# Kernel optimization log

Hardware: AMD Instinct MI355X
Metric: run time of the kernel (lower is better)

Reference implementation:

```python
import jax, jax.numpy as jnp
import numpy as np

B, S, H, NH, T = 128, 512, 768, 8, 20
HD = H // NH


def setup_inputs() -> dict:
    key = jax.random.key(0)
    ks = jax.random.split(key, 16)
    f32 = jnp.float32
    def W(i, *shape):
        return jax.random.normal(ks[i], shape, f32) * 0.02
    inp = {}
    inp["ehs"] = jax.random.normal(ks[0], (B, S, H), f32)
    inp["relevance"] = jax.random.uniform(ks[1], (B, 1), dtype=f32)
    inp["threshold"] = jnp.array([0.5], f32)
    # text_to_caption_proj: Linear, LeakyReLU, LayerNorm, Linear
    inp["tW1"] = W(2, H, H); inp["tb1"] = jnp.zeros((H,), f32)
    inp["tg"] = jnp.ones((H,), f32); inp["tbe"] = jnp.zeros((H,), f32)
    inp["tW2"] = W(3, H, H); inp["tb2"] = jnp.zeros((H,), f32)
    # image_to_caption_proj
    inp["iW1"] = W(4, H, H); inp["ib1"] = jnp.zeros((H,), f32)
    inp["ig"] = jnp.ones((H,), f32); inp["ibe"] = jnp.zeros((H,), f32)
    inp["iW2"] = W(5, H, H); inp["ib2"] = jnp.zeros((H,), f32)
    # nn.MultiheadAttention packed in_proj [3H,H] + out_proj [H,H], x2
    inp["taWin"] = W(6, 3 * H, H); inp["taBin"] = jnp.zeros((3 * H,), f32)
    inp["taWout"] = W(7, H, H); inp["taBout"] = jnp.zeros((H,), f32)
    inp["iaWin"] = W(8, 3 * H, H); inp["iaBin"] = jnp.zeros((3 * H,), f32)
    inp["iaWout"] = W(9, H, H); inp["iaBout"] = jnp.zeros((H,), f32)
    # length_adapter: Linear, LayerNorm, ReLU
    inp["laW"] = W(10, H, H); inp["laB"] = jnp.zeros((H,), f32)
    inp["laG"] = jnp.ones((H,), f32); inp["laBe"] = jnp.zeros((H,), f32)
    # quality_estimator: Linear(H,H/2), LayerNorm, ReLU, Linear(H/2,1), Sigmoid
    inp["qW1"] = W(11, H // 2, H); inp["qB1"] = jnp.zeros((H // 2,), f32)
    inp["qG"] = jnp.ones((H // 2,), f32); inp["qBe"] = jnp.zeros((H // 2,), f32)
    inp["qW2"] = W(12, 1, H // 2); inp["qB2"] = jnp.zeros((1,), f32)
    # masks: first half = text tokens, second half = image tokens; no valid
    # image caption => torch loop gives batch_max_length=0 => target_length=20
    pos = jnp.arange(S)
    inp["sentence_mask"] = jnp.tile((pos < S // 2).astype(jnp.int32)[None], (B, 1))
    inp["image_mask"] = jnp.tile((pos >= S // 2).astype(jnp.int32)[None], (B, 1))
    inp["image_caption_mask"] = jnp.zeros((B, S), jnp.int32)
    inp["image_caption_valid"] = jnp.zeros((B,), jnp.int32)
    return inp


def _ln(x, g, b, eps=1e-5):
    m = x.mean(-1, keepdims=True)
    v = ((x - m) ** 2).mean(-1, keepdims=True)
    return (x - m) / jnp.sqrt(v + eps) * g + b


def _mha(q, k, v, Win, bIn, Wout, bOut, key_pad):
    # torch nn.MultiheadAttention, batch_first=True
    Wq, Wk, Wv = jnp.split(Win, 3, axis=0)
    bq, bk, bv = jnp.split(bIn, 3, axis=0)
    def heads(x, Wp, bp):  # [B,L,H] -> [B,NH,L,HD]
        return (x @ Wp.T + bp).reshape(x.shape[0], x.shape[1], NH, HD).transpose(0, 2, 1, 3)
    qh, kh, vh = heads(q, Wq, bq), heads(k, Wk, bk), heads(v, Wv, bv)
    scores = jnp.einsum('bhqd,bhkd->bhqk', qh, kh) / jnp.sqrt(jnp.float32(HD))
    scores = jnp.where(key_pad[:, None, None, :], -1e9, scores)
    attn = jax.nn.softmax(scores, axis=-1)
    out = jnp.einsum('bhqk,bhkd->bhqd', attn, vh)
    out = out.transpose(0, 2, 1, 3).reshape(q.shape[0], q.shape[1], H)
    return out @ Wout.T + bOut


def _sinusoid_pe():
    # vectorized replacement of the scalar double for-loop
    pos = jnp.arange(T, dtype=jnp.float32)[:, None]            # [T,1]
    i = jnp.arange(0, H, 2, dtype=jnp.float32)                 # [H/2]
    ang = pos / (10000.0 ** (i / H))                           # [T,H/2]
    pe = jnp.zeros((T, H), jnp.float32)
    pe = pe.at[:, 0::2].set(jnp.sin(ang)).at[:, 1::2].set(jnp.cos(ang))
    return pe[None]  # [1,T,H]


def reference(ehs, relevance, threshold,
              tW1, tb1, tg, tbe, tW2, tb2,
              iW1, ib1, ig, ibe, iW2, ib2,
              taWin, taBin, taWout, taBout,
              iaWin, iaBin, iaWout, iaBout,
              laW, laB, laG, laBe,
              qW1, qB1, qG, qBe, qW2, qB2,
              sentence_mask, image_mask, image_caption_mask, image_caption_valid):
    sm = sentence_mask.astype(jnp.float32)[..., None]   # [B,S,1]
    im = image_mask.astype(jnp.float32)[..., None]
    text_emb = ehs * sm
    image_emb = ehs * im
    # image_caption_valid is all False => target_length = min(20, max_length-2) = T (static)
    text_len = jnp.clip(sm.sum(axis=1), 1e-9)            # [B,1]
    img_len = jnp.clip(im.sum(axis=1), 1e-9)
    text_pooled = (text_emb * sm).sum(axis=1) / text_len  # mask applied twice, as in torch
    image_pooled = (image_emb * im).sum(axis=1) / img_len
    def proj(x, W1, b1, g, be, W2, b2):
        h = jax.nn.leaky_relu(x @ W1.T + b1, 0.01)
        return _ln(h, g, be) @ W2.T + b2
    text_seed = proj(text_pooled, tW1, tb1, tg, tbe, tW2, tb2)
    image_seed = proj(image_pooled, iW1, ib1, ig, ibe, iW2, ib2)
    alpha = relevance                                     # relevance_score provided
    caption_seed = alpha * image_seed + (1.0 - alpha) * text_seed
    query = caption_seed[:, None, :] + _sinusoid_pe()     # [B,T,H]
    text_cap = _mha(query, text_emb, text_emb, taWin, taBin, taWout, taBout, sentence_mask == 0)
    image_cap = _mha(query, image_emb, image_emb, iaWin, iaBin, iaWout, iaBout, image_mask == 0)
    beta = relevance[:, :, None]                          # [B,1,1]
    cap = beta * image_cap + (1.0 - beta) * text_cap
    cap = jax.nn.relu(_ln(cap @ laW.T + laB, laG, laBe))  # length_adapter
    m = cap.mean(axis=1)
    h = jax.nn.relu(_ln(m @ qW1.T + qB1, qG, qBe))
    quality = jax.nn.sigmoid(h @ qW2.T + qB2)             # [B,1]
    return cap, quality
```

## Files before the change

### kernel.cpp

```cpp
#include <hip/hip_runtime.h>
#include <hip/hip_bf16.h>
#include <math.h>

#define B_  128
#define S_  512
#define H_  768
#define NH_ 8
#define T_  20
#define HD_ 96

typedef unsigned short u16;
typedef unsigned int   u32;

typedef __attribute__((ext_vector_type(8))) short bhalf8;
typedef __attribute__((ext_vector_type(4))) float f32x4;

union U8 { bhalf8 s; u32 u[4]; };

__device__ __forceinline__ f32x4 mfma16(bhalf8 a, bhalf8 b, f32x4 c){
  return __builtin_amdgcn_mfma_f32_16x16x32_bf16(a, b, c, 0, 0, 0);
}
__device__ __forceinline__ u32 cvtpk(float lo, float hi){
  u32 r; asm volatile("v_cvt_pk_bf16_f32 %0, %1, %2" : "=v"(r) : "v"(lo), "v"(hi));
  return r;
}
__device__ __forceinline__ float wsum(float v){
  #pragma unroll
  for(int o=32;o;o>>=1) v += __shfl_xor(v,o);
  return v;
}
__device__ __forceinline__ u16 f2bf(float f){
  u32 u = __float_as_uint(f);
  u32 r = (u + 0x7fffu + ((u>>16)&1u)) >> 16;
  return (u16)r;
}
__device__ __forceinline__ float bf2f(u32 bits){
  return __uint_as_float(bits<<16);
}

__global__ void k_cvt(const float* __restrict__ src, u16* __restrict__ dst, int n2){
  int i = blockIdx.x*256 + threadIdx.x;
  if(i < n2){
    u32 r = cvtpk(src[2*i], src[2*i+1]);
    *(u32*)(dst + 2*i) = r;
  }
}

__global__ __launch_bounds__(256) void k_prep(const float* __restrict__ ehs,
                                              u16* __restrict__ ehs_b,
                                              u16* __restrict__ ehsT){
  int blk = blockIdx.x;
  int b  = blk / 96;
  int r  = blk % 96;
  int sb = r / 12, hb = r % 12;
  int s0 = sb*64, h0 = hb*64;
  __shared__ float tile[64][65];
  int t = threadIdx.x;
  const float* src = ehs + ((size_t)b*S_ + s0)*H_ + h0;
  #pragma unroll
  for(int p2=0;p2<4;p2++){
    int row = p2*16 + (t>>4);
    int c4  = (t&15)*4;
    float4 v = *(const float4*)(src + (size_t)row*H_ + c4);
    tile[row][c4+0]=v.x; tile[row][c4+1]=v.y; tile[row][c4+2]=v.z; tile[row][c4+3]=v.w;
    u32 lo = cvtpk(v.x, v.y), hi2 = cvtpk(v.z, v.w);
    u32* dst = (u32*)(ehs_b + ((size_t)b*S_ + s0 + row)*H_ + h0 + c4);
    dst[0]=lo; dst[1]=hi2;
  }
  __syncthreads();
  #pragma unroll
  for(int p2=0;p2<4;p2++){
    int hr = p2*16 + (t>>4);
    int sg = (t&15)*4;
    float a0 = tile[sg+0][hr], a1 = tile[sg+1][hr];
    float a2 = tile[sg+2][hr], a3 = tile[sg+3][hr];
    u32 lo = cvtpk(a0,a1), hi2 = cvtpk(a2,a3);
    u32* dst = (u32*)(ehsT + ((size_t)b*H_ + h0 + hr)*S_ + s0 + sg);
    dst[0]=lo; dst[1]=hi2;
  }
}

__global__ void k_wkt(const float* __restrict__ taWin, const float* __restrict__ iaWin,
                      u16* __restrict__ WkT){
  int blk = blockIdx.x; int mha = blk/576; int t = blk%576;
  const float* Wk = (mha? iaWin : taWin) + (size_t)H_*H_;
  int bx = t%24, by = t/24;
  __shared__ float tile[32][33];
  int tx = threadIdx.x & 31, ty = threadIdx.x >> 5;
  for(int rr=ty; rr<32; rr+=8) tile[rr][tx] = Wk[(size_t)(by*32+rr)*H_ + bx*32+tx];
  __syncthreads();
  u16* dst = WkT + (size_t)mha*H_*H_;
  for(int rr=ty; rr<32; rr+=8) dst[(size_t)(bx*32+rr)*H_ + by*32+tx] = f2bf(tile[tx][rr]);
}

__global__ void k_pool(const float* __restrict__ ehs, const int* __restrict__ sm,
                       const int* __restrict__ im, u16* __restrict__ pt_b, u16* __restrict__ pi_b){
  int blk = blockIdx.x; int b = blk/3; int c0 = (blk%3)*256;
  int tid = threadIdx.x;
  __shared__ float smf[S_], imf[S_];
  for(int s=tid;s<S_;s+=256){ smf[s]=(float)sm[b*S_+s]; imf[s]=(float)im[b*S_+s]; }
  __syncthreads();
  float tl=0.f, il=0.f;
  for(int s=0;s<S_;s++){ tl+=smf[s]; il+=imf[s]; }
  tl = fmaxf(tl, 1e-9f); il = fmaxf(il, 1e-9f);
  int col = c0 + tid;
  const float* base = ehs + (size_t)b*S_*H_ + col;
  float ts=0.f, is=0.f;
  for(int s=0;s<S_;s++){
    float a = base[(size_t)s*H_];
    ts += a*smf[s];
    is += a*imf[s];
  }
  pt_b[b*H_+col] = f2bf(ts/tl);
  pi_b[b*H_+col] = f2bf(is/il);
}

__global__ __launch_bounds__(512) void k_seed(const u16* __restrict__ x_b,
                                              const u16* __restrict__ W1_b,
                                              const float* __restrict__ b1,
                                              const float* __restrict__ g,
                                              const float* __restrict__ be,
                                              const u16* __restrict__ W2_b,
                                              const float* __restrict__ b2,
                                              float* __restrict__ out){
  int row0 = blockIdx.x*16;
  int tid = threadIdx.x, lane = tid&63, w = tid>>6;
  __shared__ u16 ln[16][772];
  f32x4 acc[6];
  #pragma unroll
  for(int j=0;j<6;j++) acc[j] = (f32x4){0.f,0.f,0.f,0.f};
  for(int kt=0;kt<24;kt++){
    int ko = kt*32 + (lane>>4)*8;
    bhalf8 a = *(const bhalf8*)(x_b + (size_t)(row0 + (lane&15))*H_ + ko);
    bhalf8 bb[6];
    #pragma unroll
    for(int j=0;j<6;j++){
      int row = (w*6+j)*16 + (lane&15);
      bb[j] = *(const bhalf8*)(W1_b + (size_t)row*H_ + ko);
    }
    #pragma unroll
    for(int j=0;j<6;j++) acc[j] = mfma16(a, bb[j], acc[j]);
  }
  #pragma unroll
  for(int j=0;j<6;j++){
    int c = (w*6+j)*16 + (lane&15);
    float bv = b1[c];
    #pragma unroll
    for(int rr=0;rr<4;rr++){
      int r = (lane>>4)*4 + rr;
      float v = acc[j][rr] + bv;
      ln[r][c] = f2bf((v>=0.f)? v : 0.01f*v);
    }
  }
  __syncthreads();
  for(int ri=0; ri<2; ri++){
    int r = w*2 + ri;
    float v[12]; float s = 0.f;
    #pragma unroll
    for(int i=0;i<12;i++){ v[i] = bf2f(ln[r][lane + 64*i]); s += v[i]; }
    s = wsum(s);
    float mean = s/(float)H_;
    float pv = 0.f;
    #pragma unroll
    for(int i=0;i<12;i++){ float d = v[i]-mean; pv += d*d; }
    pv = wsum(pv);
    float rstd = rsqrtf(pv/(float)H_ + 1e-5f);
    #pragma unroll
    for(int i=0;i<12;i++){
      int c = lane + 64*i;
      ln[r][c] = f2bf((v[i]-mean)*rstd*g[c] + be[c]);
    }
  }
  __syncthreads();
  f32x4 o[6];
  #pragma unroll
  for(int j=0;j<6;j++) o[j] = (f32x4){0.f,0.f,0.f,0.f};
  for(int kt=0;kt<24;kt++){
    int ko = kt*32 + (lane>>4)*8;
    bhalf8 a = *(const bhalf8*)(&ln[lane&15][ko]);
    bhalf8 bb[6];
    #pragma unroll
    for(int j=0;j<6;j++){
      int row = (w*6+j)*16 + (lane&15);
      bb[j] = *(const bhalf8*)(W2_b + (size_t)row*H_ + ko);
    }
    #pragma unroll
    for(int j=0;j<6;j++) o[j] = mfma16(a, bb[j], o[j]);
  }
  #pragma unroll
  for(int j=0;j<6;j++){
    int c = (w*6+j)*16 + (lane&15);
    float bv = b2[c];
    #pragma unroll
    for(int rr=0;rr<4;rr++){
      int r = (lane>>4)*4 + rr;
      out[(size_t)(row0 + r)*H_ + c] = o[j][rr] + bv;
    }
  }
}

__global__ void k_query(const float* __restrict__ st, const float* __restrict__ si,
                        const float* __restrict__ rel, u16* __restrict__ query_b){
  int b = blockIdx.x; int tid = threadIdx.x;
  float a = rel[b];
  const float c = 9.210340371976184f/(float)H_;
  for(int t=0;t<32;t++){
    for(int h=tid;h<H_;h+=256){
      float val = 0.f;
      if(t < T_){
        float ang = (float)t * __expf(-(float)(h & ~1) * c);
        float pe  = (h&1)? __cosf(ang) : __sinf(ang);
        val = a*si[b*H_+h] + (1.f-a)*st[b*H_+h] + pe;
      }
      query_b[(size_t)b*32*H_ + t*H_ + h] = f2bf(val);
    }
  }
}

__global__ __launch_bounds__(512) void k_qh(const u16* __restrict__ query_b,
                                            const u16* __restrict__ Wq_b,
                                            const float* __restrict__ taBin,
                                            const float* __restrict__ iaBin,
                                            u16* __restrict__ qh_b){
  int gb = blockIdx.x; int b = gb>>1, mha = gb&1;
  int tid = threadIdx.x, lane = tid&63, w = tid>>6;
  const u16* Q  = query_b + (size_t)b*32*H_;
  const u16* Wq = Wq_b + (size_t)mha*H_*H_;
  const float* bIn = mha? iaBin : taBin;
  u16* out = qh_b + (size_t)gb*32*H_;
  f32x4 acc[2][6];
  #pragma unroll
  for(int i=0;i<2;i++)
    #pragma unroll
    for(int j=0;j<6;j++) acc[i][j] = (f32x4){0.f,0.f,0.f,0.f};
  for(int kt=0;kt<24;kt++){
    int ko = kt*32 + (lane>>4)*8;
    bhalf8 a[2];
    #pragma unroll
    for(int mt=0;mt<2;mt++)
      a[mt] = *(const bhalf8*)(Q + (size_t)(mt*16 + (lane&15))*H_ + ko);
    bhalf8 bb[6];
    #pragma unroll
    for(int j=0;j<6;j++){
      int row = (w*6+j)*16 + (lane&15);
      bb[j] = *(const bhalf8*)(Wq + (size_t)row*H_ + ko);
    }
    #pragma unroll
    for(int mt=0;mt<2;mt++)
      #pragma unroll
      for(int j=0;j<6;j++) acc[mt][j] = mfma16(a[mt], bb[j], acc[mt][j]);
  }
  #pragma unroll
  for(int mt=0;mt<2;mt++)
    #pragma unroll
    for(int j=0;j<6;j++){
      int col = (w*6+j)*16 + (lane&15);
      float bq = bIn[col];
      #pragma unroll
      for(int rr=0;rr<4;rr++){
        int row = mt*16 + (lane>>4)*4 + rr;
        out[(size_t)row*H_ + col] = f2bf(acc[mt][j][rr] + bq);
      }
    }
}

__global__ __launch_bounds__(512) void k_u(const u16* __restrict__ qh_b,
                                           const u16* __restrict__ WkT,
                                           const float* __restrict__ taBin,
                                           const float* __restrict__ iaBin,
                                           u16* __restrict__ U_b,
                                           float* __restrict__ bias_ws){
  int gb = blockIdx.x; int mha = gb&1;
  int tid = threadIdx.x, lane = tid&63, w = tid>>6;
  const u16* qh = qh_b + (size_t)gb*32*H_;
  const u16* Wk = WkT + (size_t)mha*H_*H_;
  u16* Up = U_b + (size_t)gb*160*H_;
  const float rscale = 0.10206207261596577f;
  for(int h=0; h<8; h++){
    int hd0 = h*HD_;
    for(int jn=0; jn<6; jn++){
      int nb = (w*6+jn)*16 + (lane&15);
      bhalf8 bb[3];
      #pragma unroll
      for(int kt=0;kt<3;kt++)
        bb[kt] = *(const bhalf8*)(Wk + (size_t)nb*H_ + hd0 + kt*32 + (lane>>4)*8);
      #pragma unroll
      for(int mt=0; mt<2; mt++){
        bhalf8 a[3];
        #pragma unroll
        for(int kt=0;kt<3;kt++){
          int trow = mt*16 + (lane&15);
          a[kt] = *(const bhalf8*)(qh + (size_t)trow*H_ + hd0 + kt*32 + (lane>>4)*8);
        }
        f32x4 acc = (f32x4){0.f,0.f,0.f,0.f};
        #pragma unroll
        for(int kt=0;kt<3;kt++) acc = mfma16(a[kt], bb[kt], acc);
        #pragma unroll
        for(int rr=0;rr<4;rr++){
          int trow = mt*16 + (lane>>4)*4 + rr;
          if(trow < T_)
            Up[(size_t)(h*T_+trow)*H_ + nb] = f2bf(acc[rr]*rscale);
        }
      }
    }
  }
  if(tid < 160){
    int h = tid/T_, t = tid%T_; int hd0 = h*HD_;
    const float* bIn = mha? iaBin : taBin;
    float p = 0.f;
    for(int d=0; d<HD_; d++)
      p += bf2f(qh[(size_t)t*H_ + hd0 + d]) * bIn[H_ + hd0 + d];
    bias_ws[gb*160 + tid] = p*rscale;
  }
}

__global__ __launch_bounds__(512,4) void k_scores2(const u16* __restrict__ ehs_b,
                                                   const u16* __restrict__ U_b,
                                                   const float* __restrict__ bias_ws,
                                                   const int* __restrict__ smask,
                                                   const int* __restrict__ imask,
                                                   u16* __restrict__ P_b){
  int g = blockIdx.x;
  int x = g & 7, sl = g >> 3;
  int b = x*16 + (sl>>2);
  int var = sl & 3; int mha = var>>1, rhalf = var&1;
  int gb = 2*b + mha;
  const int* msk = mha? imask : smask;
  int tid = threadIdx.x, lane = tid&63, w = tid>>6;
  int rbase = rhalf*80;
  __shared__ float sbias[80];
  __shared__ float pmax[80][8];
  __shared__ float psum[80][8];
  __shared__ float mfin[80], sinv[80];
  __shared__ u16 pst[16][520];
  if(tid < 80) sbias[tid] = bias_ws[gb*160 + rbase + tid];
  __syncthreads();
  const u16* Ub = U_b + (size_t)gb*160*H_;
  const u16* Eb = ehs_b + (size_t)b*S_*H_;
  bool mk[4];
  #pragma unroll
  for(int j=0;j<4;j++) mk[j] = msk[b*S_ + w*64 + j*16 + (lane&15)] != 0;

  f32x4 acc[5][4];
  #pragma unroll
  for(int i=0;i<5;i++)
    #pragma unroll
    for(int j=0;j<4;j++) acc[i][j] = (f32x4){0.f,0.f,0.f,0.f};
  for(int kt=0;kt<24;kt++){
    int ko = kt*32 + (lane>>4)*8;
    bhalf8 a[5];
    #pragma unroll
    for(int i=0;i<5;i++)
      a[i] = *(const bhalf8*)(Ub + (size_t)(rbase + i*16 + (lane&15))*H_ + ko);
    bhalf8 bb[4];
    #pragma unroll
    for(int j=0;j<4;j++)
      bb[j] = *(const bhalf8*)(Eb + (size_t)(w*64 + j*16 + (lane&15))*H_ + ko);
    #pragma unroll
    for(int i=0;i<5;i++)
      #pragma unroll
      for(int j=0;j<4;j++) acc[i][j] = mfma16(a[i], bb[j], acc[i][j]);
  }
  #pragma unroll
  for(int i=0;i<5;i++)
    #pragma unroll
    for(int rr=0;rr<4;rr++){
      int row = i*16 + (lane>>4)*4 + rr;
      float bias = sbias[row];
      float vmax = -3e38f;
      #pragma unroll
      for(int j=0;j<4;j++){
        float v = acc[i][j][rr] + bias;
        acc[i][j][rr] = v;
        if(mk[j]) vmax = fmaxf(vmax, v);
      }
      #pragma unroll
      for(int o=1;o<16;o<<=1) vmax = fmaxf(vmax, __shfl_xor(vmax,o));
      if((lane&15)==0) pmax[row][w] = vmax;
    }
  __syncthreads();
  if(tid < 80){
    float m = pmax[tid][0];
    #pragma unroll
    for(int ww=1;ww<8;ww++) m = fmaxf(m, pmax[tid][ww]);
    mfin[tid] = m;
  }
  __syncthreads();
  #pragma unroll
  for(int i=0;i<5;i++)
    #pragma unroll
    for(int rr=0;rr<4;rr++){
      int row = i*16 + (lane>>4)*4 + rr;
      float m = mfin[row];
      float ssum = 0.f;
      #pragma unroll
      for(int j=0;j<4;j++){
        float e = mk[j]? __expf(acc[i][j][rr] - m) : 0.f;
        acc[i][j][rr] = e;
        ssum += e;
      }
      #pragma unroll
      for(int o=1;o<16;o<<=1) ssum += __shfl_xor(ssum,o);
      if((lane&15)==0) psum[row][w] = ssum;
    }
  __syncthreads();
  if(tid < 80){
    float ss = 0.f;
    #pragma unroll
    for(int ww=0;ww<8;ww++) ss += psum[tid][ww];
    sinv[tid] = 1.f/ss;
  }
  __syncthreads();
  u16* Pp = P_b + (size_t)gb*160*S_ + (size_t)rbase*S_;
  for(int i=0;i<5;i++){
    #pragma unroll
    for(int rr=0;rr<4;rr++){
      int r16 = (lane>>4)*4 + rr;
      float inv = sinv[i*16 + r16];
      #pragma unroll
      for(int j=0;j<4;j++){
        int col = w*64 + j*16 + (lane&15);
        pst[r16][col] = f2bf(acc[i][j][rr]*inv);
      }
    }
    __syncthreads();
    for(int e=tid; e<16*256; e+=512){
      int r16 = e>>8, c = e&255;
      u32 v = *(const u32*)&pst[r16][2*c];
      *(u32*)(Pp + (size_t)(i*16 + r16)*S_ + 2*c) = v;
    }
    __syncthreads();
  }
}

__global__ __launch_bounds__(512) void k_ctx2(const u16* __restrict__ ehsT,
                                              const u16* __restrict__ P_b,
                                              u16* __restrict__ ctx_b){
  int blk = blockIdx.x; int b = blk>>1, nh = blk&1;
  int tid = threadIdx.x, lane = tid&63, w = tid>>6;
  __shared__ u16 ct[80][392];
  int nbase = nh*384 + w*48;
  for(int mha=0; mha<2; mha++){
    const u16* Pp = P_b + (size_t)(2*b+mha)*160*S_;
    f32x4 acc[10][3];
    #pragma unroll
    for(int i=0;i<10;i++)
      #pragma unroll
      for(int j=0;j<3;j++) acc[i][j] = (f32x4){0.f,0.f,0.f,0.f};
    for(int kt=0;kt<16;kt++){
      int ko = kt*32 + (lane>>4)*8;
      bhalf8 bb[3];
      #pragma unroll
      for(int t2=0;t2<3;t2++){
        int n = nbase + t2*16 + (lane&15);
        bb[t2] = *(const bhalf8*)(ehsT + ((size_t)b*H_ + n)*S_ + ko);
      }
      bhalf8 a[10];
      #pragma unroll
      for(int i=0;i<10;i++){
        int row = i*16 + (lane&15);
        a[i] = *(const bhalf8*)(Pp + (size_t)row*S_ + ko);
      }
      #pragma unroll
      for(int i=0;i<10;i++)
        #pragma unroll
        for(int t2=0;t2<3;t2++) acc[i][t2] = mfma16(a[i], bb[t2], acc[i][t2]);
    }
    u16* Cp = ctx_b + (size_t)(2*b+mha)*160*H_ + nh*384;
    #pragma unroll
    for(int half=0; half<2; half++){
      __syncthreads();
      #pragma unroll
      for(int i=0;i<5;i++)
        #pragma unroll
        for(int t2=0;t2<3;t2++)
          #pragma unroll
          for(int rr=0;rr<4;rr++){
            int rloc = i*16 + (lane>>4)*4 + rr;
            int cl = w*48 + t2*16 + (lane&15);
            ct[rloc][cl] = f2bf(acc[half*5+i][t2][rr]);
          }
      __syncthreads();
      for(int e=tid; e<80*192; e+=512){
        int r = e/192, c2 = (e%192)*2;
        u32 v = (u32)ct[r][c2] | ((u32)ct[r][c2+1]<<16);
        *(u32*)(Cp + (size_t)(half*80 + r)*H_ + c2) = v;
      }
    }
    __syncthreads();
  }
}

__global__ __launch_bounds__(512) void k_out(const u16* __restrict__ ctx_b,
                                             const u16* __restrict__ Wv_b,
                                             const u16* __restrict__ Wo_b,
                                             const float* __restrict__ taBin,
                                             const float* __restrict__ iaBin,
                                             float* __restrict__ out_t,
                                             float* __restrict__ out_i){
  int gb = blockIdx.x; int b = gb>>1, mha = gb&1;
  int tid = threadIdx.x, lane = tid&63, w = tid>>6;
  const float* bIn = mha? iaBin : taBin;
  const u16* Wv = Wv_b + (size_t)mha*H_*H_;
  const u16* Wo = Wo_b + (size_t)mha*H_*H_;
  const u16* Cp = ctx_b + (size_t)gb*160*H_;
  __shared__ u16 vt[32][784];
  int hd0 = w*HD_;
  {
    f32x4 acc[2][6];
    #pragma unroll
    for(int i=0;i<2;i++)
      #pragma unroll
      for(int j=0;j<6;j++) acc[i][j] = (f32x4){0.f,0.f,0.f,0.f};
    for(int kt=0;kt<24;kt++){
      int ko = kt*32 + (lane>>4)*8;
      bhalf8 a[2];
      #pragma unroll
      for(int mt=0;mt<2;mt++){
        int trow = mt*16 + (lane&15);
        a[mt] = *(const bhalf8*)(Cp + (size_t)(w*T_ + trow)*H_ + ko);
      }
      bhalf8 bb[6];
      #pragma unroll
      for(int j=0;j<6;j++){
        int row = hd0 + j*16 + (lane&15);
        bb[j] = *(const bhalf8*)(Wv + (size_t)row*H_ + ko);
      }
      #pragma unroll
      for(int mt=0;mt<2;mt++)
        #pragma unroll
        for(int j=0;j<6;j++) acc[mt][j] = mfma16(a[mt], bb[j], acc[mt][j]);
    }
    #pragma unroll
    for(int mt=0;mt<2;mt++)
      #pragma unroll
      for(int j=0;j<6;j++){
        int col = j*16 + (lane&15);
        float bv = bIn[2*H_ + hd0 + col];
        #pragma unroll
        for(int rr=0;rr<4;rr++){
          int trow = mt*16 + (lane>>4)*4 + rr;
          vt[trow][hd0 + col] = f2bf(acc[mt][j][rr] + bv);
        }
      }
  }
  __syncthreads();
  {
    f32x4 o[2][6];
    #pragma unroll
    for(int i=0;i<2;i++)
      #pragma unroll
      for(int j=0;j<6;j++) o[i][j] = (f32x4){0.f,0.f,0.f,0.f};
    for(int kt=0;kt<24;kt++){
      int ko = kt*32 + (lane>>4)*8;
      bhalf8 a[2];
      #pragma unroll
      for(int mt=0;mt<2;mt++)
        a[mt] = *(const bhalf8*)(&vt[mt*16 + (lane&15)][ko]);
      bhalf8 bb[6];
      #pragma unroll
      for(int j=0;j<6;j++){
        int row = (w*6+j)*16 + (lane&15);
        bb[j] = *(const bhalf8*)(Wo + (size_t)row*H_ + ko);
      }
      #pragma unroll
      for(int mt=0;mt<2;mt++)
        #pragma unroll
        for(int j=0;j<6;j++) o[mt][j] = mfma16(a[mt], bb[j], o[mt][j]);
    }
    float* op = (mha? out_i : out_t) + (size_t)b*T_*H_;
    #pragma unroll
    for(int mt=0;mt<2;mt++)
      #pragma unroll
      for(int j=0;j<6;j++){
        int col = (w*6+j)*16 + (lane&15);
        #pragma unroll
        for(int rr=0;rr<4;rr++){
          int trow = mt*16 + (lane>>4)*4 + rr;
          if(trow < T_) op[(size_t)trow*H_ + col] = o[mt][j][rr];
        }
      }
  }
}

__global__ void k_comb(const float* __restrict__ out_t, const float* __restrict__ out_i,
                       const float* __restrict__ taBout, const float* __restrict__ iaBout,
                       const float* __restrict__ rel, u16* __restrict__ comb_b){
  int bt = blockIdx.x; int b = bt/T_;
  float beta = rel[b];
  for(int h=threadIdx.x; h<H_; h+=256){
    float vt = out_t[(size_t)bt*H_+h] + taBout[h];
    float vi = out_i[(size_t)bt*H_+h] + iaBout[h];
    comb_b[(size_t)bt*H_+h] = f2bf(beta*vi + (1.f-beta)*vt);
  }
}

__global__ __launch_bounds__(512) void k_cap2(const u16* __restrict__ comb_b,
                                              const u16* __restrict__ laW_b,
                                              const float* __restrict__ laB,
                                              const float* __restrict__ laG,
                                              const float* __restrict__ laBe,
                                              float* __restrict__ cap){
  int blk = blockIdx.x; int row0 = blk*16;
  int tid = threadIdx.x, lane = tid&63, w = tid>>6;
  __shared__ float sy[16][776];
  f32x4 acc[6];
  #pragma unroll
  for(int j=0;j<6;j++) acc[j] = (f32x4){0.f,0.f,0.f,0.f};
  for(int kt=0;kt<24;kt++){
    int ko = kt*32 + (lane>>4)*8;
    bhalf8 a = *(const bhalf8*)(comb_b + (size_t)(row0 + (lane&15))*H_ + ko);
    bhalf8 bb[6];
    #pragma unroll
    for(int j=0;j<6;j++){
      int row = (w*6+j)*16 + (lane&15);
      bb[j] = *(const bhalf8*)(laW_b + (size_t)row*H_ + ko);
    }
    #pragma unroll
    for(int j=0;j<6;j++) acc[j] = mfma16(a, bb[j], acc[j]);
  }
  #pragma unroll
  for(int j=0;j<6;j++){
    int c = (w*6+j)*16 + (lane&15);
    float lb = laB[c];
    #pragma unroll
    for(int rr=0;rr<4;rr++){
      int r = (lane>>4)*4 + rr;
      sy[r][c] = acc[j][rr] + lb;
    }
  }
  __syncthreads();
  for(int ri=0; ri<2; ri++){
    int r = w*2 + ri;
    float v[12];
    float s = 0.f;
    #pragma unroll
    for(int i=0;i<12;i++){ v[i] = sy[r][lane + 64*i]; s += v[i]; }
    s = wsum(s);
    float mean = s/(float)H_;
    float pv = 0.f;
    #pragma unroll
    for(int i=0;i<12;i++){ float d = v[i]-mean; pv += d*d; }
    pv = wsum(pv);
    float rstd = rsqrtf(pv/(float)H_ + 1e-5f);
    float* cp = cap + (size_t)(row0 + r)*H_;
    #pragma unroll
    for(int i=0;i<12;i++){
      int c = lane + 64*i;
      float o = (v[i]-mean)*rstd*laG[c] + laBe[c];
      cp[c] = (o>0.f)? o : 0.f;
    }
  }
}

__global__ __launch_bounds__(512) void k_quality2(const float* __restrict__ cap,
                                                  const u16* __restrict__ qW1_b,
                                                  const float* __restrict__ qB1,
                                                  const float* __restrict__ qG,
                                                  const float* __restrict__ qBe,
                                                  const float* __restrict__ qW2,
                                                  const float* __restrict__ qB2,
                                                  float* __restrict__ outq){
  const int H2 = H_/2;
  int b0 = blockIdx.x*16;
  int tid = threadIdx.x, lane = tid&63, w = tid>>6;
  __shared__ u16 sm_a[16][772];
  __shared__ float sy[16][388];
  for(int e=tid; e<16*H_; e+=512){
    int r = e/H_, c = e%H_;
    const float* cp = cap + ((size_t)(b0+r)*T_)*H_ + c;
    float s = 0.f;
    #pragma unroll
    for(int t=0;t<T_;t++) s += cp[(size_t)t*H_];
    sm_a[r][c] = f2bf(s*(1.f/(float)T_));
  }
  __syncthreads();
  f32x4 acc[3];
  #pragma unroll
  for(int j=0;j<3;j++) acc[j] = (f32x4){0.f,0.f,0.f,0.f};
  for(int kt=0;kt<24;kt++){
    int ko = kt*32 + (lane>>4)*8;
    bhalf8 a = *(const bhalf8*)(&sm_a[lane&15][ko]);
    bhalf8 bb[3];
    #pragma unroll
    for(int j=0;j<3;j++){
      int row = (w*3+j)*16 + (lane&15);
      bb[j] = *(const bhalf8*)(qW1_b + (size_t)row*H_ + ko);
    }
    #pragma unroll
    for(int j=0;j<3;j++) acc[j] = mfma16(a, bb[j], acc[j]);
  }
  #pragma unroll
  for(int j=0;j<3;j++){
    int c = (w*3+j)*16 + (lane&15);
    float q1 = qB1[c];
    #pragma unroll
    for(int rr=0;rr<4;rr++){
      int r = (lane>>4)*4 + rr;
      sy[r][c] = acc[j][rr] + q1;
    }
  }
  __syncthreads();
  for(int ri=0; ri<2; ri++){
    int r = w*2 + ri;
    float v[6]; float s = 0.f;
    #pragma unroll
    for(int i=0;i<6;i++){ v[i] = sy[r][lane + 64*i]; s += v[i]; }
    s = wsum(s);
    float mean = s/(float)H2;
    float pv = 0.f;
    #pragma unroll
    for(int i=0;i<6;i++){ float d = v[i]-mean; pv += d*d; }
    pv = wsum(pv);
    float rstd = rsqrtf(pv/(float)H2 + 1e-5f);
    float dot = 0.f;
    #pragma unroll
    for(int i=0;i<6;i++){
      int c = lane + 64*i;
      float u = (v[i]-mean)*rstd*qG[c] + qBe[c];
      u = (u>0.f)? u : 0.f;
      dot += u*qW2[c];
    }
    dot = wsum(dot);
    if(lane==0){
      float z = dot + qB2[0];
      outq[b0+r] = 1.f/(1.f+__expf(-z));
    }
  }
}

extern "C" void kernel_launch(void* const* d_in, const int* in_sizes, int n_in,
                              void* d_out, int out_size, void* d_ws, size_t ws_size,
                              hipStream_t stream){
  const float* ehs    = (const float*)d_in[0];
  const float* rel    = (const float*)d_in[1];
  const float* tW1    = (const float*)d_in[3];
  const float* tb1    = (const float*)d_in[4];
  const float* tg     = (const float*)d_in[5];
  const float* tbe    = (const float*)d_in[6];
  const float* tW2    = (const float*)d_in[7];
  const float* tb2    = (const float*)d_in[8];
  const float* iW1    = (const float*)d_in[9];
  const float* ib1    = (const float*)d_in[10];
  const float* ig     = (const float*)d_in[11];
  const float* ibe    = (const float*)d_in[12];
  const float* iW2    = (const float*)d_in[13];
  const float* ib2    = (const float*)d_in[14];
  const float* taWin  = (const float*)d_in[15];
  const float* taBin  = (const float*)d_in[16];
  const float* taWout = (const float*)d_in[17];
  const float* taBout = (const float*)d_in[18];
  const float* iaWin  = (const float*)d_in[19];
  const float* iaBin  = (const float*)d_in[20];
  const float* iaWout = (const float*)d_in[21];
  const float* iaBout = (const float*)d_in[22];
  const float* laW    = (const float*)d_in[23];
  const float* laB    = (const float*)d_in[24];
  const float* laG    = (const float*)d_in[25];
  const float* laBe   = (const float*)d_in[26];
  const float* qW1    = (const float*)d_in[27];
  const float* qB1    = (const float*)d_in[28];
  const float* qG     = (const float*)d_in[29];
  const float* qBe    = (const float*)d_in[30];
  const float* qW2    = (const float*)d_in[31];
  const float* qB2    = (const float*)d_in[32];
  const int* smask    = (const int*)d_in[33];
  const int* imask    = (const int*)d_in[34];

  char* p = (char*)d_ws;
  auto take = [&](size_t bytes)->char*{
    char* r = p; p += (bytes + 255) & ~(size_t)255; return r;
  };
  float* st      = (float*)take((size_t)B_*H_*4);
  float* si      = (float*)take((size_t)B_*H_*4);
  u16*  pt_b     = (u16*)take((size_t)B_*H_*2);
  u16*  pi_b     = (u16*)take((size_t)B_*H_*2);
  u16*  query_b  = (u16*)take((size_t)B_*32*H_*2);
  u16*  qh_b     = (u16*)take((size_t)B_*2*32*H_*2);
  u16*  WkT      = (u16*)take((size_t)2*H_*H_*2);
  u16*  Wq_b     = (u16*)take((size_t)2*H_*H_*2);
  u16*  Wv_b     = (u16*)take((size_t)2*H_*H_*2);
  u16*  Wo_b     = (u16*)take((size_t)2*H_*H_*2);
  u16*  laW_b    = (u16*)take((size_t)H_*H_*2);
  u16*  tW1_b    = (u16*)take((size_t)H_*H_*2);
  u16*  tW2_b    = (u16*)take((size_t)H_*H_*2);
  u16*  iW1_b    = (u16*)take((size_t)H_*H_*2);
  u16*  iW2_b    = (u16*)take((size_t)H_*H_*2);
  u16*  qW1_b    = (u16*)take((size_t)(H_/2)*H_*2);
  float* bias_ws = (float*)take((size_t)B_*2*160*4);
  u16*  U_b      = (u16*)take((size_t)B_*2*160*H_*2);
  u16*  P_b      = (u16*)take((size_t)B_*2*160*S_*2);
  float* out_t   = (float*)take((size_t)B_*T_*H_*4);
  float* out_i   = (float*)take((size_t)B_*T_*H_*4);
  u16*  comb_b   = (u16*)take((size_t)B_*T_*H_*2);
  u16*  ehs_b    = (u16*)take((size_t)B_*S_*H_*2);
  u16*  ehsT     = (u16*)take((size_t)B_*H_*S_*2);
  u16*  ctx_b    = U_b;

  const int nW2 = (H_*H_)/2;
  const int cvtg = (nW2 + 255)/256;
  const int nQ2 = ((H_/2)*H_)/2;
  const int cvtgq = (nQ2 + 255)/256;

  hipLaunchKernelGGL(k_prep, dim3(B_*96), dim3(256), 0, stream, ehs, ehs_b, ehsT);

  hipLaunchKernelGGL(k_cvt, dim3(cvtg), dim3(256), 0, stream, taWin,              Wq_b,           nW2);
  hipLaunchKernelGGL(k_cvt, dim3(cvtg), dim3(256), 0, stream, iaWin,              Wq_b + (size_t)H_*H_, nW2);
  hipLaunchKernelGGL(k_cvt, dim3(cvtg), dim3(256), 0, stream, taWin + 2*H_*H_,    Wv_b,           nW2);
  hipLaunchKernelGGL(k_cvt, dim3(cvtg), dim3(256), 0, stream, iaWin + 2*H_*H_,    Wv_b + (size_t)H_*H_, nW2);
  hipLaunchKernelGGL(k_cvt, dim3(cvtg), dim3(256), 0, stream, taWout,             Wo_b,           nW2);
  hipLaunchKernelGGL(k_cvt, dim3(cvtg), dim3(256), 0, stream, iaWout,             Wo_b + (size_t)H_*H_, nW2);
  hipLaunchKernelGGL(k_cvt, dim3(cvtg), dim3(256), 0, stream, laW,                laW_b,          nW2);
  hipLaunchKernelGGL(k_cvt, dim3(cvtg), dim3(256), 0, stream, tW1,                tW1_b,          nW2);
  hipLaunchKernelGGL(k_cvt, dim3(cvtg), dim3(256), 0, stream, tW2,                tW2_b,          nW2);
  hipLaunchKernelGGL(k_cvt, dim3(cvtg), dim3(256), 0, stream, iW1,                iW1_b,          nW2);
  hipLaunchKernelGGL(k_cvt, dim3(cvtg), dim3(256), 0, stream, iW2,                iW2_b,          nW2);
  hipLaunchKernelGGL(k_cvt, dim3(cvtgq), dim3(256), 0, stream, qW1,               qW1_b,          nQ2);
  hipLaunchKernelGGL(k_wkt, dim3(1152), dim3(256), 0, stream, taWin, iaWin, WkT);

  hipLaunchKernelGGL(k_pool,  dim3(B_*3), dim3(256), 0, stream, ehs, smask, imask, pt_b, pi_b);
  hipLaunchKernelGGL(k_seed,  dim3(B_/16), dim3(512), 0, stream, pt_b, tW1_b, tb1, tg, tbe, tW2_b, tb2, st);
  hipLaunchKernelGGL(k_seed,  dim3(B_/16), dim3(512), 0, stream, pi_b, iW1_b, ib1, ig, ibe, iW2_b, ib2, si);
  hipLaunchKernelGGL(k_query, dim3(B_),   dim3(256), 0, stream, st, si, rel, query_b);

  hipLaunchKernelGGL(k_qh,      dim3(B_*2),  dim3(512), 0, stream, query_b, Wq_b, taBin, iaBin, qh_b);
  hipLaunchKernelGGL(k_u,       dim3(B_*2),  dim3(512), 0, stream, qh_b, WkT, taBin, iaBin, U_b, bias_ws);
  hipLaunchKernelGGL(k_scores2, dim3(B_*4),  dim3(512), 0, stream, ehs_b, U_b, bias_ws, smask, imask, P_b);
  hipLaunchKernelGGL(k_ctx2,    dim3(B_*2),  dim3(512), 0, stream, ehsT, P_b, ctx_b);
  hipLaunchKernelGGL(k_out,     dim3(B_*2),  dim3(512), 0, stream, ctx_b, Wv_b, Wo_b, taBin, iaBin, out_t, out_i);

  float* cap = (float*)d_out;
  hipLaunchKernelGGL(k_comb, dim3(B_*T_), dim3(256), 0, stream, out_t, out_i, taBout, iaBout, rel, comb_b);
  hipLaunchKernelGGL(k_cap2, dim3((B_*T_)/16), dim3(512), 0, stream, comb_b, laW_b, laB, laG, laBe, cap);
  hipLaunchKernelGGL(k_quality2, dim3(B_/16), dim3(512), 0, stream,
                     cap, qW1_b, qB1, qG, qBe, qW2, qB2, cap + (size_t)B_*T_*H_);
}
```

Before: 836.7 us.

## Fuse combine into length adapter, split ctx blocks, stage U stores, pool from bf16

Several independent changes. The pooling kernel now reads the bf16 copy of ehs instead of fp32, halving its memory traffic at a small precision cost. k_u stages each head's output in shared memory so global stores go out as coalesced 32-bit row writes instead of scattered 16-bit ones. k_ctx2 launches one block per (batch, half, mha) with an XCD-aware batch mapping, doubling the grid for parallelism. The k_comb kernel is removed and its beta-weighted bias add is folded into the length-adapter GEMM's A-operand load, which removes an intermediate buffer and one launch.

```diff
diff --git a/kernel.cpp b/kernel.cpp
--- a/kernel.cpp
+++ b/kernel.cpp
@@ -93,7 +93,7 @@
   for(int rr=ty; rr<32; rr+=8) dst[(size_t)(bx*32+rr)*H_ + by*32+tx] = f2bf(tile[tx][rr]);
 }
 
-__global__ void k_pool(const float* __restrict__ ehs, const int* __restrict__ sm,
+__global__ void k_pool(const u16* __restrict__ ehs_b, const int* __restrict__ sm,
                        const int* __restrict__ im, u16* __restrict__ pt_b, u16* __restrict__ pi_b){
   int blk = blockIdx.x; int b = blk/3; int c0 = (blk%3)*256;
   int tid = threadIdx.x;
@@ -104,10 +104,10 @@
   for(int s=0;s<S_;s++){ tl+=smf[s]; il+=imf[s]; }
   tl = fmaxf(tl, 1e-9f); il = fmaxf(il, 1e-9f);
   int col = c0 + tid;
-  const float* base = ehs + (size_t)b*S_*H_ + col;
+  const u16* base = ehs_b + (size_t)b*S_*H_ + col;
   float ts=0.f, is=0.f;
   for(int s=0;s<S_;s++){
-    float a = base[(size_t)s*H_];
+    float a = bf2f(base[(size_t)s*H_]);
     ts += a*smf[s];
     is += a*imf[s];
   }
@@ -275,6 +275,7 @@
   const u16* qh = qh_b + (size_t)gb*32*H_;
   const u16* Wk = WkT + (size_t)mha*H_*H_;
   u16* Up = U_b + (size_t)gb*160*H_;
+  __shared__ u16 ut[20][776];
   const float rscale = 0.10206207261596577f;
   for(int h=0; h<8; h++){
     int hd0 = h*HD_;
@@ -299,10 +300,17 @@
         for(int rr=0;rr<4;rr++){
           int trow = mt*16 + (lane>>4)*4 + rr;
           if(trow < T_)
-            Up[(size_t)(h*T_+trow)*H_ + nb] = f2bf(acc[rr]*rscale);
+            ut[trow][nb] = f2bf(acc[rr]*rscale);
         }
       }
     }
+    __syncthreads();
+    for(int e=tid; e<20*384; e+=512){
+      int r = e/384, c2 = (e%384)*2;
+      u32 v = *(const u32*)&ut[r][c2];
+      *(u32*)(Up + (size_t)(h*T_ + r)*H_ + c2) = v;
+    }
+    __syncthreads();
   }
   if(tid < 160){
     int h = tid/T_, t = tid%T_; int hd0 = h*HD_;
@@ -436,58 +444,58 @@
 __global__ __launch_bounds__(512) void k_ctx2(const u16* __restrict__ ehsT,
                                               const u16* __restrict__ P_b,
                                               u16* __restrict__ ctx_b){
-  int blk = blockIdx.x; int b = blk>>1, nh = blk&1;
+  int g = blockIdx.x;
+  int x = g & 7, sl = g >> 3;
+  int b = x*16 + (sl>>2);
+  int var = sl & 3; int nh = var>>1, mha = var&1;
   int tid = threadIdx.x, lane = tid&63, w = tid>>6;
   __shared__ u16 ct[80][392];
   int nbase = nh*384 + w*48;
-  for(int mha=0; mha<2; mha++){
-    const u16* Pp = P_b + (size_t)(2*b+mha)*160*S_;
-    f32x4 acc[10][3];
+  const u16* Pp = P_b + (size_t)(2*b+mha)*160*S_;
+  f32x4 acc[10][3];
+  #pragma unroll
+  for(int i=0;i<10;i++)
+    #pragma unroll
+    for(int j=0;j<3;j++) acc[i][j] = (f32x4){0.f,0.f,0.f,0.f};
+  for(int kt=0;kt<16;kt++){
+    int ko = kt*32 + (lane>>4)*8;
+    bhalf8 bb[3];
+    #pragma unroll
+    for(int t2=0;t2<3;t2++){
+      int n = nbase + t2*16 + (lane&15);
+      bb[t2] = *(const bhalf8*)(ehsT + ((size_t)b*H_ + n)*S_ + ko);
+    }
+    bhalf8 a[10];
+    #pragma unroll
+    for(int i=0;i<10;i++){
+      int row = i*16 + (lane&15);
+      a[i] = *(const bhalf8*)(Pp + (size_t)row*S_ + ko);
+    }
     #pragma unroll
     for(int i=0;i<10;i++)
       #pragma unroll
-      for(int j=0;j<3;j++) acc[i][j] = (f32x4){0.f,0.f,0.f,0.f};
-    for(int kt=0;kt<16;kt++){
-      int ko = kt*32 + (lane>>4)*8;
-      bhalf8 bb[3];
-      #pragma unroll
-      for(int t2=0;t2<3;t2++){
-        int n = nbase + t2*16 + (lane&15);
-        bb[t2] = *(const bhalf8*)(ehsT + ((size_t)b*H_ + n)*S_ + ko);
-      }
-      bhalf8 a[10];
-      #pragma unroll
-      for(int i=0;i<10;i++){
-        int row = i*16 + (lane&15);
-        a[i] = *(const bhalf8*)(Pp + (size_t)row*S_ + ko);
-      }
-      #pragma unroll
-      for(int i=0;i<10;i++)
+      for(int t2=0;t2<3;t2++) acc[i][t2] = mfma16(a[i], bb[t2], acc[i][t2]);
+  }
+  u16* Cp = ctx_b + (size_t)(2*b+mha)*160*H_ + nh*384;
+  #pragma unroll
+  for(int half=0; half<2; half++){
+    __syncthreads();
+    #pragma unroll
+    for(int i=0;i<5;i++)
+      #pragma unroll
+      for(int t2=0;t2<3;t2++)
         #pragma unroll
-        for(int t2=0;t2<3;t2++) acc[i][t2] = mfma16(a[i], bb[t2], acc[i][t2]);
-    }
-    u16* Cp = ctx_b + (size_t)(2*b+mha)*160*H_ + nh*384;
-    #pragma unroll
-    for(int half=0; half<2; half++){
-      __syncthreads();
-      #pragma unroll
-      for(int i=0;i<5;i++)
-        #pragma unroll
-        for(int t2=0;t2<3;t2++)
-          #pragma unroll
-          for(int rr=0;rr<4;rr++){
-            int rloc = i*16 + (lane>>4)*4 + rr;
-            int cl = w*48 + t2*16 + (lane&15);
-            ct[rloc][cl] = f2bf(acc[half*5+i][t2][rr]);
-          }
-      __syncthreads();
-      for(int e=tid; e<80*192; e+=512){
-        int r = e/192, c2 = (e%192)*2;
-        u32 v = (u32)ct[r][c2] | ((u32)ct[r][c2+1]<<16);
-        *(u32*)(Cp + (size_t)(half*80 + r)*H_ + c2) = v;
-      }
-    }
+        for(int rr=0;rr<4;rr++){
+          int rloc = i*16 + (lane>>4)*4 + rr;
+          int cl = w*48 + t2*16 + (lane&15);
+          ct[rloc][cl] = f2bf(acc[half*5+i][t2][rr]);
+        }
     __syncthreads();
+    for(int e=tid; e<80*192; e+=512){
+      int r = e/192, c2 = (e%192)*2;
+      u32 v = (u32)ct[r][c2] | ((u32)ct[r][c2+1]<<16);
+      *(u32*)(Cp + (size_t)(half*80 + r)*H_ + c2) = v;
+    }
   }
 }
 
@@ -583,19 +591,11 @@
   }
 }
 
-__global__ void k_comb(const float* __restrict__ out_t, const float* __restrict__ out_i,
-                       const float* __restrict__ taBout, const float* __restrict__ iaBout,
-                       const float* __restrict__ rel, u16* __restrict__ comb_b){
-  int bt = blockIdx.x; int b = bt/T_;
-  float beta = rel[b];
-  for(int h=threadIdx.x; h<H_; h+=256){
-    float vt = out_t[(size_t)bt*H_+h] + taBout[h];
-    float vi = out_i[(size_t)bt*H_+h] + iaBout[h];
-    comb_b[(size_t)bt*H_+h] = f2bf(beta*vi + (1.f-beta)*vt);
-  }
-}
-
-__global__ __launch_bounds__(512) void k_cap2(const u16* __restrict__ comb_b,
+__global__ __launch_bounds__(512) void k_cap3(const float* __restrict__ out_t,
+                                              const float* __restrict__ out_i,
+                                              const float* __restrict__ taBout,
+                                              const float* __restrict__ iaBout,
+                                              const float* __restrict__ rel,
                                               const u16* __restrict__ laW_b,
                                               const float* __restrict__ laB,
                                               const float* __restrict__ laG,
@@ -604,12 +604,33 @@
   int blk = blockIdx.x; int row0 = blk*16;
   int tid = threadIdx.x, lane = tid&63, w = tid>>6;
   __shared__ float sy[16][776];
+  __shared__ float sbo[H_], sbi[H_];
+  for(int j=tid;j<H_;j+=512){ sbo[j]=taBout[j]; sbi[j]=iaBout[j]; }
+  __syncthreads();
+  int arow = row0 + (lane&15);
+  float beta = rel[arow/T_];
   f32x4 acc[6];
   #pragma unroll
   for(int j=0;j<6;j++) acc[j] = (f32x4){0.f,0.f,0.f,0.f};
   for(int kt=0;kt<24;kt++){
     int ko = kt*32 + (lane>>4)*8;
-    bhalf8 a = *(const bhalf8*)(comb_b + (size_t)(row0 + (lane&15))*H_ + ko);
+    const float* tp = out_t + (size_t)arow*H_ + ko;
+    const float* ip = out_i + (size_t)arow*H_ + ko;
+    float4 t0 = *(const float4*)tp, t1 = *(const float4*)(tp+4);
+    float4 i0 = *(const float4*)ip, i1 = *(const float4*)(ip+4);
+    float v[8];
+    v[0] = beta*(i0.x+sbi[ko+0]) + (1.f-beta)*(t0.x+sbo[ko+0]);
+    v[1] = beta*(i0.y+sbi[ko+1]) + (1.f-beta)*(t0.y+sbo[ko+1]);
+    v[2] = beta*(i0.z+sbi[ko+2]) + (1.f-beta)*(t0.z+sbo[ko+2]);
+    v[3] = beta*(i0.w+sbi[ko+3]) + (1.f-beta)*(t0.w+sbo[ko+3]);
+    v[4] = beta*(i1.x+sbi[ko+4]) + (1.f-beta)*(t1.x+sbo[ko+4]);
+    v[5] = beta*(i1.y+sbi[ko+5]) + (1.f-beta)*(t1.y+sbo[ko+5]);
+    v[6] = beta*(i1.z+sbi[ko+6]) + (1.f-beta)*(t1.z+sbo[ko+6]);
+    v[7] = beta*(i1.w+sbi[ko+7]) + (1.f-beta)*(t1.w+sbo[ko+7]);
+    U8 u;
+    u.u[0]=cvtpk(v[0],v[1]); u.u[1]=cvtpk(v[2],v[3]);
+    u.u[2]=cvtpk(v[4],v[5]); u.u[3]=cvtpk(v[6],v[7]);
+    bhalf8 a = u.s;
     bhalf8 bb[6];
     #pragma unroll
     for(int j=0;j<6;j++){
@@ -792,7 +813,6 @@
   u16*  P_b      = (u16*)take((size_t)B_*2*160*S_*2);
   float* out_t   = (float*)take((size_t)B_*T_*H_*4);
   float* out_i   = (float*)take((size_t)B_*T_*H_*4);
-  u16*  comb_b   = (u16*)take((size_t)B_*T_*H_*2);
   u16*  ehs_b    = (u16*)take((size_t)B_*S_*H_*2);
   u16*  ehsT     = (u16*)take((size_t)B_*H_*S_*2);
   u16*  ctx_b    = U_b;
@@ -818,7 +838,7 @@
   hipLaunchKernelGGL(k_cvt, dim3(cvtgq), dim3(256), 0, stream, qW1,               qW1_b,          nQ2);
   hipLaunchKernelGGL(k_wkt, dim3(1152), dim3(256), 0, stream, taWin, iaWin, WkT);
 
-  hipLaunchKernelGGL(k_pool,  dim3(B_*3), dim3(256), 0, stream, ehs, smask, imask, pt_b, pi_b);
+  hipLaunchKernelGGL(k_pool,  dim3(B_*3), dim3(256), 0, stream, ehs_b, smask, imask, pt_b, pi_b);
   hipLaunchKernelGGL(k_seed,  dim3(B_/16), dim3(512), 0, stream, pt_b, tW1_b, tb1, tg, tbe, tW2_b, tb2, st);
   hipLaunchKernelGGL(k_seed,  dim3(B_/16), dim3(512), 0, stream, pi_b, iW1_b, ib1, ig, ibe, iW2_b, ib2, si);
   hipLaunchKernelGGL(k_query, dim3(B_),   dim3(256), 0, stream, st, si, rel, query_b);
@@ -826,12 +846,12 @@
   hipLaunchKernelGGL(k_qh,      dim3(B_*2),  dim3(512), 0, stream, query_b, Wq_b, taBin, iaBin, qh_b);
   hipLaunchKernelGGL(k_u,       dim3(B_*2),  dim3(512), 0, stream, qh_b, WkT, taBin, iaBin, U_b, bias_ws);
   hipLaunchKernelGGL(k_scores2, dim3(B_*4),  dim3(512), 0, stream, ehs_b, U_b, bias_ws, smask, imask, P_b);
-  hipLaunchKernelGGL(k_ctx2,    dim3(B_*2),  dim3(512), 0, stream, ehsT, P_b, ctx_b);
+  hipLaunchKernelGGL(k_ctx2,    dim3(B_*4),  dim3(512), 0, stream, ehsT, P_b, ctx_b);
   hipLaunchKernelGGL(k_out,     dim3(B_*2),  dim3(512), 0, stream, ctx_b, Wv_b, Wo_b, taBin, iaBin, out_t, out_i);
 
   float* cap = (float*)d_out;
-  hipLaunchKernelGGL(k_comb, dim3(B_*T_), dim3(256), 0, stream, out_t, out_i, taBout, iaBout, rel, comb_b);
-  hipLaunchKernelGGL(k_cap2, dim3((B_*T_)/16), dim3(512), 0, stream, comb_b, laW_b, laB, laG, laBe, cap);
+  hipLaunchKernelGGL(k_cap3, dim3((B_*T_)/16), dim3(512), 0, stream,
+                     out_t, out_i, taBout, iaBout, rel, laW_b, laB, laG, laBe, cap);
   hipLaunchKernelGGL(k_quality2, dim3(B_/16), dim3(512), 0, stream,
                      cap, qW1_b, qB1, qG, qBe, qW2, qB2, cap + (size_t)B_*T_*H_);
 }
```

New measurement: 838.7 us. No clear change (+0.2%).
